# Performance work log

Measured on AMD Instinct MI355X. Metric: run time of the kernel, lower is better.

Reference implementation:

```python
import jax, jax.numpy as jnp
import numpy as np

NL, D, NH, HD, MLP, L = 4, 1280, 16, 80, 5120, 2048
SEG = 512  # patches per packed image


def setup_inputs() -> dict:
    key = jax.random.key(0)
    ks = jax.random.split(key, 16)
    s = 0.02
    # per-segment RoPE frequency table: positions restart at each image boundary
    inv_freq = 1.0 / (10000.0 ** (jnp.arange(0, HD, 2, dtype=jnp.float32) / HD))  # (HD/2,)
    pos = (jnp.arange(L) % SEG).astype(jnp.float32)
    rotary_pos_emb = pos[:, None] * inv_freq[None, :]  # (L, HD/2)
    return {
        "x": jax.random.normal(ks[0], (L, D), jnp.float32),
        "rotary_pos_emb": rotary_pos_emb,
        "cu_seqlens": jnp.array([0, 512, 1024, 1536, 2048], jnp.int32),
        "ln1_g": 1.0 + s * jax.random.normal(ks[1], (NL, D), jnp.float32),
        "ln1_b": s * jax.random.normal(ks[2], (NL, D), jnp.float32),
        "ln2_g": 1.0 + s * jax.random.normal(ks[3], (NL, D), jnp.float32),
        "ln2_b": s * jax.random.normal(ks[4], (NL, D), jnp.float32),
        "qkv_w": s * jax.random.normal(ks[5], (NL, 3 * D, D), jnp.float32),
        "qkv_b": s * jax.random.normal(ks[6], (NL, 3 * D), jnp.float32),
        "proj_w": s * jax.random.normal(ks[7], (NL, D, D), jnp.float32),
        "proj_b": s * jax.random.normal(ks[8], (NL, D), jnp.float32),
        "mlp_w1": s * jax.random.normal(ks[9], (NL, MLP, D), jnp.float32),
        "mlp_b1": s * jax.random.normal(ks[10], (NL, MLP), jnp.float32),
        "mlp_w2": s * jax.random.normal(ks[11], (NL, D, MLP), jnp.float32),
        "mlp_b2": s * jax.random.normal(ks[12], (NL, D), jnp.float32),
    }


def _ln(x, g, b):
    m = jnp.mean(x, axis=-1, keepdims=True)
    v = jnp.mean((x - m) ** 2, axis=-1, keepdims=True)
    return (x - m) * jax.lax.rsqrt(v + 1e-6) * g + b


def _rope(t, cos, sin):
    # t: (L, H, HD); cos/sin: (L, 1, HD)
    half = t.shape[-1] // 2
    rot = jnp.concatenate([-t[..., half:], t[..., :half]], axis=-1)
    return t * cos + rot * sin


def reference(x, rotary_pos_emb, cu_seqlens, ln1_g, ln1_b, ln2_g, ln2_b,
              qkv_w, qkv_b, proj_w, proj_b, mlp_w1, mlp_b1, mlp_w2, mlp_b2):
    Lx = x.shape[0]
    cos = jnp.cos(rotary_pos_emb)
    sin = jnp.sin(rotary_pos_emb)
    cos = jnp.concatenate([cos, cos], axis=-1)[:, None, :]  # (L,1,HD)
    sin = jnp.concatenate([sin, sin], axis=-1)[:, None, :]
    # block-diagonal attention mask from cu_seqlens via segment ids
    seg = jnp.searchsorted(cu_seqlens, jnp.arange(Lx), side="right")  # (L,)
    mask = seg[:, None] == seg[None, :]  # (L,L) bool
    neg = jnp.finfo(jnp.float32).min
    scale = 1.0 / np.sqrt(HD)
    for l in range(qkv_w.shape[0]):
        h = _ln(x, ln1_g[l], ln1_b[l])
        qkv = (h @ qkv_w[l].T + qkv_b[l]).reshape(Lx, 3, NH, HD)
        q, k, v = qkv[:, 0], qkv[:, 1], qkv[:, 2]  # (L,H,HD) each
        q = _rope(q, cos, sin)
        k = _rope(k, cos, sin)
        scores = jnp.einsum("lhd,mhd->hlm", q, k) * scale  # (H,L,L)
        scores = jnp.where(mask[None], scores, neg)
        w = jax.nn.softmax(scores.astype(jnp.float32), axis=-1).astype(x.dtype)
        att = jnp.einsum("hlm,mhd->lhd", w, v).reshape(Lx, NH * HD)
        x = x + att @ proj_w[l].T + proj_b[l]
        h = _ln(x, ln2_g[l], ln2_b[l])
        x = x + jax.nn.gelu(h @ mlp_w1[l].T + mlp_b1[l], approximate=True) @ mlp_w2[l].T + mlp_b2[l]
    return x
```

## Files before the change

kernel.cpp:

```cpp
#include <hip/hip_runtime.h>
#include <cstdint>
#include <cstddef>

typedef unsigned short u16;
typedef __bf16 bf16_t;
typedef bf16_t bf16x8 __attribute__((ext_vector_type(8)));
typedef float f32x4 __attribute__((ext_vector_type(4)));

#define NLAY 4
#define DMODEL 1280
#define NHEAD 16
#define HDIM 80
#define HDP 96
#define MLPD 5120
#define LTOK 2048
#define SEGLEN 512

__device__ __forceinline__ u16 f2bf(float f) {
  union { float f; unsigned u; } x; x.f = f;
  unsigned r = x.u + 0x7fffu + ((x.u >> 16) & 1u);
  return (u16)(r >> 16);
}
__device__ __forceinline__ float bf2f(u16 s) {
  union { unsigned u; float f; } x; x.u = ((unsigned)s) << 16;
  return x.f;
}

#define GLOAD_LDS16(gsrc, ldst) \
  __builtin_amdgcn_global_load_lds((const __attribute__((address_space(1))) void*)(gsrc), \
                                   (__attribute__((address_space(3))) void*)(ldst), 16, 0, 0)

__device__ __forceinline__ void barrier_mem() {
  asm volatile("s_barrier" ::: "memory");
}

#define C0 (3 * DMODEL * DMODEL / 4)
#define C1 (C0 + DMODEL * DMODEL / 4)
#define C2 (C1 + MLPD * DMODEL / 4)
#define C3 (C2 + DMODEL * MLPD / 4)
__global__ __launch_bounds__(256) void cvt4(const float* __restrict__ s_q,
                                            const float* __restrict__ s_p,
                                            const float* __restrict__ s_1,
                                            const float* __restrict__ s_2,
                                            u16* __restrict__ o_q, u16* __restrict__ o_p,
                                            u16* __restrict__ o_1, u16* __restrict__ o_2) {
  int i = blockIdx.x * 256 + threadIdx.x;
  const float* src; u16* dst; int off;
  if (i < C0)      { src = s_q; dst = o_q; off = i; }
  else if (i < C1) { src = s_p; dst = o_p; off = i - C0; }
  else if (i < C2) { src = s_1; dst = o_1; off = i - C1; }
  else if (i < C3) { src = s_2; dst = o_2; off = i - C2; }
  else return;
  const float4 v = reinterpret_cast<const float4*>(src)[off];
  union { u16 s[4]; uint2 u; } o;
  o.s[0] = f2bf(v.x); o.s[1] = f2bf(v.y); o.s[2] = f2bf(v.z); o.s[3] = f2bf(v.w);
  reinterpret_cast<uint2*>(dst)[off] = o.u;
}

__global__ __launch_bounds__(256) void ln_bf16(const float* __restrict__ x,
                                               const float* __restrict__ g,
                                               const float* __restrict__ b,
                                               u16* __restrict__ out) {
  int row = blockIdx.x;
  int t = threadIdx.x;
  const float* xr = x + (size_t)row * DMODEL;
  float v[5]; float s = 0.f, s2 = 0.f;
#pragma unroll
  for (int i = 0; i < 5; i++) { v[i] = xr[t + i * 256]; s += v[i]; s2 += v[i] * v[i]; }
#pragma unroll
  for (int off = 32; off; off >>= 1) { s += __shfl_down(s, off); s2 += __shfl_down(s2, off); }
  __shared__ float ps[4], ps2[4];
  int w = t >> 6;
  if ((t & 63) == 0) { ps[w] = s; ps2[w] = s2; }
  __syncthreads();
  s = ps[0] + ps[1] + ps[2] + ps[3];
  s2 = ps2[0] + ps2[1] + ps2[2] + ps2[3];
  float mean = s * (1.f / DMODEL);
  float var = s2 * (1.f / DMODEL) - mean * mean;
  float inv = rsqrtf(var + 1e-6f);
#pragma unroll
  for (int i = 0; i < 5; i++) {
    int c = t + i * 256;
    out[(size_t)row * DMODEL + c] = f2bf((v[i] - mean) * inv * g[c] + b[c]);
  }
}

template <int EPI>
__global__ __launch_bounds__(512, 4) void gemmhp(const u16* __restrict__ A,
                                                 const u16* __restrict__ B,
                                                 const float* __restrict__ bias,
                                                 u16* __restrict__ Cb,
                                                 int M, int N, int K) {
  __shared__ u16 As[3][128 * 32];
  __shared__ u16 Bs[3][256 * 32];

  int gN = gridDim.x, gM = gridDim.y;
  int flat = blockIdx.x + gN * blockIdx.y;
  int nwg = gN * gM;
  int qc = nwg >> 3, rc = nwg & 7;
  int xcd = flat & 7, pos = flat >> 3;
  int start = (xcd < rc) ? xcd * (qc + 1) : rc * (qc + 1) + (xcd - rc) * qc;
  int swz = start + pos;
  int m0 = (swz % gM) * 128;
  int n0 = (swz / gM) * 256;

  int t = threadIdx.x, lane = t & 63, w = t >> 6;
  int wm = w >> 2, wn = w & 3;
  int r = lane & 15, kq = lane >> 4;
  f32x4 acc[4][4] = {};

  auto stageA = [&](int buf, int k0) {
    int row = t >> 2, s = t & 3;
    int ss = s ^ ((row >> 1) & 3);
    GLOAD_LDS16(A + (size_t)(m0 + row) * K + k0 + ss * 8, &As[buf][t * 8]);
  };
  auto stageB = [&](int buf, int k0) {
#pragma unroll
    for (int i = 0; i < 2; i++) {
      int chunk = i * 512 + t;
      int row = chunk >> 2, s = chunk & 3;
      int ss = s ^ ((row >> 1) & 3);
      GLOAD_LDS16(B + (size_t)(n0 + row) * K + k0 + ss * 8, &Bs[buf][chunk * 8]);
    }
  };

  int NT = K >> 5;
  stageA(0, 0); stageB(0, 0);
  stageA(1, 32); stageB(1, 32);

  int bt = 0;
  for (int kt = 0; kt < NT; kt++) {
    if (kt == NT - 1) asm volatile("s_waitcnt vmcnt(0)" ::: "memory");
    else              asm volatile("s_waitcnt vmcnt(3)" ::: "memory");
    barrier_mem();
    const u16* as = As[bt];
    const u16* bs = Bs[bt];
    int b2 = bt + 2; if (b2 >= 3) b2 -= 3;
    bool st = (kt + 2) < NT;
    int k2 = (kt + 2) << 5;

    bf16x8 af[4], bfv[4];
#pragma unroll
    for (int i = 0; i < 4; i++) {
      int row = wm * 64 + i * 16 + r;
      int ss = kq ^ ((row >> 1) & 3);
      af[i] = *(const bf16x8*)&as[row * 32 + ss * 8];
    }
#pragma unroll
    for (int j = 0; j < 4; j++) {
      int row = wn * 64 + j * 16 + r;
      int ss = kq ^ ((row >> 1) & 3);
      bfv[j] = *(const bf16x8*)&bs[row * 32 + ss * 8];
    }
    if (st) { stageA(b2, k2); stageB(b2, k2); }
    __builtin_amdgcn_s_setprio(1);
#pragma unroll
    for (int i = 0; i < 4; i++)
#pragma unroll
      for (int j = 0; j < 4; j++)
        acc[i][j] = __builtin_amdgcn_mfma_f32_16x16x32_bf16(af[i], bfv[j], acc[i][j], 0, 0, 0);
    __builtin_amdgcn_s_setprio(0);

    bt++; if (bt == 3) bt = 0;
  }

#pragma unroll
  for (int i = 0; i < 4; i++) {
#pragma unroll
    for (int j = 0; j < 4; j++) {
      int col = n0 + wn * 64 + j * 16 + r;
      float bv = bias[col];
#pragma unroll
      for (int reg = 0; reg < 4; reg++) {
        int rowg = m0 + wm * 64 + i * 16 + kq * 4 + reg;
        float val = acc[i][j][reg] + bv;
        if (EPI == 2) {
          float z2 = -1.5957691216057308f * fmaf(0.044715f * val, val * val, val);
          float gg = val / (1.f + __expf(z2));
          Cb[(size_t)rowg * N + col] = f2bf(gg);
        } else {
          Cb[(size_t)rowg * N + col] = f2bf(val);
        }
      }
    }
  }
}

template <int EPI>
__global__ __launch_bounds__(256, 3) void gemmdp(const u16* __restrict__ A,
                                                 const u16* __restrict__ B,
                                                 const float* __restrict__ bias,
                                                 float* __restrict__ Cf,
                                                 int M, int N, int K) {
  __shared__ u16 As[3][128 * 32];
  __shared__ u16 Bs[3][128 * 32];

  int gN = gridDim.x, gM = gridDim.y;
  int flat = blockIdx.x + gN * blockIdx.y;
  int nwg = gN * gM;
  int qc = nwg >> 3, rc = nwg & 7;
  int xcd = flat & 7, pos = flat >> 3;
  int start = (xcd < rc) ? xcd * (qc + 1) : rc * (qc + 1) + (xcd - rc) * qc;
  int swz = start + pos;
  int m0 = (swz % gM) * 128;
  int n0 = (swz / gM) * 128;

  int t = threadIdx.x, lane = t & 63, w = t >> 6;
  int wm = w >> 1, wn = w & 1;
  int r = lane & 15, kq = lane >> 4;
  f32x4 acc[4][4] = {};

  auto stage = [&](int buf, int k0) {
#pragma unroll
    for (int i = 0; i < 2; i++) {
      int chunk = i * 256 + t;
      int row = chunk >> 2, s = chunk & 3;
      int ss = s ^ ((row >> 1) & 3);
      GLOAD_LDS16(A + (size_t)(m0 + row) * K + k0 + ss * 8, &As[buf][chunk * 8]);
    }
#pragma unroll
    for (int i = 0; i < 2; i++) {
      int chunk = i * 256 + t;
      int row = chunk >> 2, s = chunk & 3;
      int ss = s ^ ((row >> 1) & 3);
      GLOAD_LDS16(B + (size_t)(n0 + row) * K + k0 + ss * 8, &Bs[buf][chunk * 8]);
    }
  };

  int NT = K >> 5;
  stage(0, 0);
  stage(1, 32);

  int bt = 0;
  for (int kt = 0; kt < NT; kt++) {
    if (kt == NT - 1) asm volatile("s_waitcnt vmcnt(0)" ::: "memory");
    else              asm volatile("s_waitcnt vmcnt(4)" ::: "memory");
    barrier_mem();
    const u16* as = As[bt];
    const u16* bs = Bs[bt];
    int b2 = bt + 2; if (b2 >= 3) b2 -= 3;
    bool st = (kt + 2) < NT;
    int k2 = (kt + 2) << 5;

    bf16x8 af[4], bfv[4];
#pragma unroll
    for (int i = 0; i < 4; i++) {
      int row = wm * 64 + i * 16 + r;
      int ss = kq ^ ((row >> 1) & 3);
      af[i] = *(const bf16x8*)&as[row * 32 + ss * 8];
    }
#pragma unroll
    for (int j = 0; j < 4; j++) {
      int row = wn * 64 + j * 16 + r;
      int ss = kq ^ ((row >> 1) & 3);
      bfv[j] = *(const bf16x8*)&bs[row * 32 + ss * 8];
    }
    if (st) stage(b2, k2);
    __builtin_amdgcn_s_setprio(1);
#pragma unroll
    for (int i = 0; i < 4; i++)
#pragma unroll
      for (int j = 0; j < 4; j++)
        acc[i][j] = __builtin_amdgcn_mfma_f32_16x16x32_bf16(af[i], bfv[j], acc[i][j], 0, 0, 0);
    __builtin_amdgcn_s_setprio(0);

    bt++; if (bt == 3) bt = 0;
  }

#pragma unroll
  for (int i = 0; i < 4; i++) {
#pragma unroll
    for (int j = 0; j < 4; j++) {
      int col = n0 + wn * 64 + j * 16 + r;
      float bv = bias[col];
#pragma unroll
      for (int reg = 0; reg < 4; reg++) {
        int rowg = m0 + wm * 64 + i * 16 + kq * 4 + reg;
        Cf[(size_t)rowg * N + col] += acc[i][j][reg] + bv;
      }
    }
  }
}

__global__ __launch_bounds__(256) void rope_pack(const u16* __restrict__ qkv,
                                                 const float* __restrict__ rpe,
                                                 u16* __restrict__ qp,
                                                 u16* __restrict__ kp) {
  int l = blockIdx.x;
  int t = threadIdx.x;
  __shared__ float cs[40], sn[40];
  if (t < 40) {
    float a = rpe[l * 40 + t];
    cs[t] = cosf(a);
    sn[t] = sinf(a);
  }
  __syncthreads();
  const u16* row = qkv + (size_t)l * (3 * DMODEL);
  const float scale = 0.11180339887498949f;
#pragma unroll
  for (int i = 0; i < 5; i++) {
    int e = t + i * 256;
    int h = e / HDIM, d = e - h * HDIM;
    int dm = (d < 40) ? d : d - 40;
    float c = cs[dm], s = sn[dm];
    float qv = bf2f(row[h * HDIM + d]);
    float qr = (d < 40) ? -bf2f(row[h * HDIM + d + 40]) : bf2f(row[h * HDIM + d - 40]);
    qp[((size_t)h * LTOK + l) * HDP + d] = f2bf((qv * c + qr * s) * scale);
    float kv = bf2f(row[DMODEL + h * HDIM + d]);
    float kr = (d < 40) ? -bf2f(row[DMODEL + h * HDIM + d + 40]) : bf2f(row[DMODEL + h * HDIM + d - 40]);
    kp[((size_t)h * LTOK + l) * HDP + d] = f2bf(kv * c + kr * s);
  }
  {
    int h = t >> 4, p = t & 15;
    qp[((size_t)h * LTOK + l) * HDP + HDIM + p] = 0;
    kp[((size_t)h * LTOK + l) * HDP + HDIM + p] = 0;
  }
}

__global__ __launch_bounds__(256) void vtrans(const u16* __restrict__ qkv,
                                              u16* __restrict__ vt) {
  int blk = blockIdx.x;
  int h = blk >> 5, lt = blk & 31;
  int t = threadIdx.x;
  __shared__ u16 ld[64][81];
#pragma unroll
  for (int i = 0; i < 20; i++) {
    int idx = t + i * 256;
    int ll = idx / HDIM, d = idx - ll * HDIM;
    ld[ll][d] = qkv[(size_t)(lt * 64 + ll) * (3 * DMODEL) + 2 * DMODEL + h * HDIM + d];
  }
  __syncthreads();
#pragma unroll
  for (int i = 0; i < 20; i++) {
    int idx = t + i * 256;
    int d = idx >> 6, ll = idx & 63;
    vt[((size_t)h * HDIM + d) * LTOK + lt * 64 + ll] = ld[ll][d];
  }
}

__global__ __launch_bounds__(256) void attn(const u16* __restrict__ qp,
                                            const u16* __restrict__ kp,
                                            const u16* __restrict__ vt,
                                            u16* __restrict__ out) {
  int bid = blockIdx.x;
  int h = bid >> 5;
  int seg = (bid >> 3) & 3;
  int qt = bid & 7;
  int t = threadIdx.x, w = t >> 6, lane = t & 63;
  int r = lane & 15, kq = lane >> 4;
  __shared__ u16 P[4][16][512];
  int seg0 = seg * SEGLEN;
  int q0 = seg0 + qt * 64 + w * 16;

  bf16x8 qf[3];
  const u16* qrow = qp + ((size_t)h * LTOK + q0 + r) * HDP;
#pragma unroll
  for (int kk = 0; kk < 3; kk++) qf[kk] = *(const bf16x8*)(qrow + kk * 32 + kq * 8);

  f32x4 sc[32];
#pragma unroll
  for (int j = 0; j < 32; j++) {
    f32x4 a = {0.f, 0.f, 0.f, 0.f};
    const u16* krow = kp + ((size_t)h * LTOK + seg0 + j * 16 + r) * HDP;
#pragma unroll
    for (int kk = 0; kk < 3; kk++) {
      bf16x8 bfr = *(const bf16x8*)(krow + kk * 32 + kq * 8);
      a = __builtin_amdgcn_mfma_f32_16x16x32_bf16(qf[kk], bfr, a, 0, 0, 0);
    }
    sc[j] = a;
  }

#pragma unroll
  for (int rr = 0; rr < 4; rr++) {
    float m = -1e30f;
#pragma unroll
    for (int j = 0; j < 32; j++) m = fmaxf(m, sc[j][rr]);
#pragma unroll
    for (int off = 1; off < 16; off <<= 1) m = fmaxf(m, __shfl_xor(m, off));
    float s = 0.f;
#pragma unroll
    for (int j = 0; j < 32; j++) { float e = __expf(sc[j][rr] - m); sc[j][rr] = e; s += e; }
#pragma unroll
    for (int off = 1; off < 16; off <<= 1) s += __shfl_xor(s, off);
    float inv = 1.f / s;
#pragma unroll
    for (int j = 0; j < 32; j++)
      P[w][kq * 4 + rr][j * 16 + r] = f2bf(sc[j][rr] * inv);
  }
  __syncthreads();

  f32x4 oc[5] = {};
#pragma unroll
  for (int tt = 0; tt < 16; tt++) {
    bf16x8 a = *(const bf16x8*)&P[w][r][tt * 32 + kq * 8];
#pragma unroll
    for (int n = 0; n < 5; n++) {
      const u16* vrow = vt + ((size_t)h * HDIM + n * 16 + r) * LTOK + seg0 + tt * 32 + kq * 8;
      bf16x8 bfr = *(const bf16x8*)vrow;
      oc[n] = __builtin_amdgcn_mfma_f32_16x16x32_bf16(a, bfr, oc[n], 0, 0, 0);
    }
  }
#pragma unroll
  for (int n = 0; n < 5; n++)
#pragma unroll
    for (int reg = 0; reg < 4; reg++) {
      int l = q0 + kq * 4 + reg;
      out[(size_t)l * DMODEL + h * HDIM + n * 16 + r] = f2bf(oc[n][reg]);
    }
}

extern "C" void kernel_launch(void* const* d_in, const int* in_sizes, int n_in,
                              void* d_out, int out_size, void* d_ws, size_t ws_size,
                              hipStream_t stream) {
  (void)in_sizes; (void)n_in; (void)out_size; (void)ws_size;
  const float* x_in   = (const float*)d_in[0];
  const float* rpe    = (const float*)d_in[1];
  const float* ln1_g  = (const float*)d_in[3];
  const float* ln1_b  = (const float*)d_in[4];
  const float* ln2_g  = (const float*)d_in[5];
  const float* ln2_b  = (const float*)d_in[6];
  const float* qkv_w  = (const float*)d_in[7];
  const float* qkv_b  = (const float*)d_in[8];
  const float* proj_w = (const float*)d_in[9];
  const float* proj_b = (const float*)d_in[10];
  const float* mlp_w1 = (const float*)d_in[11];
  const float* mlp_b1 = (const float*)d_in[12];
  const float* mlp_w2 = (const float*)d_in[13];
  const float* mlp_b2 = (const float*)d_in[14];
  float* x = (float*)d_out;

  char* ws = (char*)d_ws;
  size_t off = 0;
  auto alloc = [&](size_t bytes) -> char* {
    char* p = ws + off;
    off = (off + bytes + 255) & ~(size_t)255;
    return p;
  };
  u16* wq  = (u16*)alloc((size_t)3 * DMODEL * DMODEL * 2);
  u16* wp  = (u16*)alloc((size_t)DMODEL * DMODEL * 2);
  u16* w1  = (u16*)alloc((size_t)MLPD * DMODEL * 2);
  u16* w2  = (u16*)alloc((size_t)DMODEL * MLPD * 2);
  u16* hb  = (u16*)alloc((size_t)LTOK * DMODEL * 2);
  u16* qkvb = (u16*)alloc((size_t)LTOK * 3 * DMODEL * 2);
  u16* qp  = (u16*)alloc((size_t)NHEAD * LTOK * HDP * 2);
  u16* kp  = (u16*)alloc((size_t)NHEAD * LTOK * HDP * 2);
  u16* vt  = (u16*)alloc((size_t)NHEAD * HDIM * LTOK * 2);
  u16* att = (u16*)alloc((size_t)LTOK * DMODEL * 2);
  u16* ge  = (u16*)alloc((size_t)LTOK * MLPD * 2);

  hipMemcpyAsync(x, x_in, (size_t)LTOK * DMODEL * sizeof(float),
                 hipMemcpyDeviceToDevice, stream);

  for (int l = 0; l < NLAY; l++) {
    cvt4<<<(C3 + 255) / 256, 256, 0, stream>>>(
        qkv_w + (size_t)l * 3 * DMODEL * DMODEL, proj_w + (size_t)l * DMODEL * DMODEL,
        mlp_w1 + (size_t)l * MLPD * DMODEL, mlp_w2 + (size_t)l * DMODEL * MLPD,
        wq, wp, w1, w2);

    ln_bf16<<<LTOK, 256, 0, stream>>>(x, ln1_g + l * DMODEL, ln1_b + l * DMODEL, hb);
    gemmhp<3><<<dim3(15, 16), 512, 0, stream>>>(
        hb, wq, qkv_b + (size_t)l * 3 * DMODEL, qkvb, LTOK, 3 * DMODEL, DMODEL);
    rope_pack<<<LTOK, 256, 0, stream>>>(qkvb, rpe, qp, kp);
    vtrans<<<NHEAD * 32, 256, 0, stream>>>(qkvb, vt);
    attn<<<NHEAD * 4 * 8, 256, 0, stream>>>(qp, kp, vt, att);
    gemmdp<1><<<dim3(10, 16), 256, 0, stream>>>(
        att, wp, proj_b + (size_t)l * DMODEL, x, LTOK, DMODEL, DMODEL);
    ln_bf16<<<LTOK, 256, 0, stream>>>(x, ln2_g + l * DMODEL, ln2_b + l * DMODEL, hb);
    gemmhp<2><<<dim3(20, 16), 512, 0, stream>>>(
        hb, w1, mlp_b1 + (size_t)l * MLPD, ge, LTOK, MLPD, DMODEL);
    gemmdp<1><<<dim3(10, 16), 256, 0, stream>>>(
        ge, w2, mlp_b2 + (size_t)l * DMODEL, x, LTOK, DMODEL, MLPD);
  }
}
```

Before: 1.078 ms.

## Split-K the projection and MLP-down GEMMs with bf16 partials and a reduce kernel

Replaces the residual-accumulating GEMM used for the attention projection and the MLP down-projection with a split-K variant. It launches 4 K-slices per tile, so 640 workgroups run instead of 160 on a 256-CU part. Each slice writes its partial sums as bf16 into reused scratch buffers (the ge region, and the hb region spilling into qkvb). A separate vectorised kernel then sums the four partials, adds the bias and updates the fp32 residual. The cost is extra memory traffic and one more launch per GEMM, plus reduced precision because the partials are rounded to bf16 before summation.

New measurement: 927.7 us. -13.9%, faster.

```diff
diff --git a/kernel.cpp b/kernel.cpp
--- a/kernel.cpp
+++ b/kernel.cpp
@@ -186,12 +186,10 @@
   }
 }
 
-template <int EPI>
-__global__ __launch_bounds__(256, 3) void gemmdp(const u16* __restrict__ A,
-                                                 const u16* __restrict__ B,
-                                                 const float* __restrict__ bias,
-                                                 float* __restrict__ Cf,
-                                                 int M, int N, int K) {
+__global__ __launch_bounds__(256, 3) void gemmskb(const u16* __restrict__ A,
+                                                  const u16* __restrict__ B,
+                                                  u16* __restrict__ P,
+                                                  int M, int N, int K, int KC) {
   __shared__ u16 As[3][128 * 32];
   __shared__ u16 Bs[3][128 * 32];
 
@@ -204,6 +202,8 @@
   int swz = start + pos;
   int m0 = (swz % gM) * 128;
   int n0 = (swz / gM) * 128;
+  int kbase = blockIdx.z * KC;
+  u16* Pz = P + (size_t)blockIdx.z * M * N;
 
   int t = threadIdx.x, lane = t & 63, w = t >> 6;
   int wm = w >> 1, wn = w & 1;
@@ -227,9 +227,9 @@
     }
   };
 
-  int NT = K >> 5;
-  stage(0, 0);
-  stage(1, 32);
+  int NT = KC >> 5;
+  stage(0, kbase);
+  stage(1, kbase + 32);
 
   int bt = 0;
   for (int kt = 0; kt < NT; kt++) {
@@ -240,7 +240,7 @@
     const u16* bs = Bs[bt];
     int b2 = bt + 2; if (b2 >= 3) b2 -= 3;
     bool st = (kt + 2) < NT;
-    int k2 = (kt + 2) << 5;
+    int k2 = kbase + ((kt + 2) << 5);
 
     bf16x8 af[4], bfv[4];
 #pragma unroll
@@ -272,14 +272,39 @@
 #pragma unroll
     for (int j = 0; j < 4; j++) {
       int col = n0 + wn * 64 + j * 16 + r;
-      float bv = bias[col];
 #pragma unroll
       for (int reg = 0; reg < 4; reg++) {
         int rowg = m0 + wm * 64 + i * 16 + kq * 4 + reg;
-        Cf[(size_t)rowg * N + col] += acc[i][j][reg] + bv;
+        Pz[(size_t)rowg * N + col] = f2bf(acc[i][j][reg]);
       }
     }
   }
+}
+
+#define N8TOT (LTOK * DMODEL / 8)
+__global__ __launch_bounds__(256) void reduce4b(const u16* __restrict__ P,
+                                                const float* __restrict__ bias,
+                                                float4* __restrict__ x) {
+  int i = blockIdx.x * 256 + threadIdx.x;
+  if (i >= N8TOT) return;
+  const size_t PS = (size_t)LTOK * DMODEL;
+  float s[8] = {};
+#pragma unroll
+  for (int z = 0; z < 4; z++) {
+    uint4 pv = *reinterpret_cast<const uint4*>(P + z * PS + (size_t)i * 8);
+    const u16* ps = (const u16*)&pv;
+#pragma unroll
+    for (int e = 0; e < 8; e++) s[e] += bf2f(ps[e]);
+  }
+  int cb = (i % (DMODEL / 8)) * 8;
+  float4 b0 = *reinterpret_cast<const float4*>(bias + cb);
+  float4 b1 = *reinterpret_cast<const float4*>(bias + cb + 4);
+  float4 xv0 = x[i * 2], xv1 = x[i * 2 + 1];
+  xv0.x += s[0] + b0.x; xv0.y += s[1] + b0.y;
+  xv0.z += s[2] + b0.z; xv0.w += s[3] + b0.w;
+  xv1.x += s[4] + b1.x; xv1.y += s[5] + b1.y;
+  xv1.z += s[6] + b1.z; xv1.w += s[7] + b1.w;
+  x[i * 2] = xv0; x[i * 2 + 1] = xv1;
 }
 
 __global__ __launch_bounds__(256) void rope_pack(const u16* __restrict__ qkv,
@@ -447,6 +472,8 @@
   u16* vt  = (u16*)alloc((size_t)NHEAD * HDIM * LTOK * 2);
   u16* att = (u16*)alloc((size_t)LTOK * DMODEL * 2);
   u16* ge  = (u16*)alloc((size_t)LTOK * MLPD * 2);
+  u16* pk_proj = ge;
+  u16* pk_mlp2 = hb;
 
   hipMemcpyAsync(x, x_in, (size_t)LTOK * DMODEL * sizeof(float),
                  hipMemcpyDeviceToDevice, stream);
@@ -463,12 +490,16 @@
     rope_pack<<<LTOK, 256, 0, stream>>>(qkvb, rpe, qp, kp);
     vtrans<<<NHEAD * 32, 256, 0, stream>>>(qkvb, vt);
     attn<<<NHEAD * 4 * 8, 256, 0, stream>>>(qp, kp, vt, att);
-    gemmdp<1><<<dim3(10, 16), 256, 0, stream>>>(
-        att, wp, proj_b + (size_t)l * DMODEL, x, LTOK, DMODEL, DMODEL);
+    gemmskb<<<dim3(10, 16, 4), 256, 0, stream>>>(
+        att, wp, pk_proj, LTOK, DMODEL, DMODEL, DMODEL / 4);
+    reduce4b<<<(N8TOT + 255) / 256, 256, 0, stream>>>(
+        pk_proj, proj_b + (size_t)l * DMODEL, (float4*)x);
     ln_bf16<<<LTOK, 256, 0, stream>>>(x, ln2_g + l * DMODEL, ln2_b + l * DMODEL, hb);
     gemmhp<2><<<dim3(20, 16), 512, 0, stream>>>(
         hb, w1, mlp_b1 + (size_t)l * MLPD, ge, LTOK, MLPD, DMODEL);
-    gemmdp<1><<<dim3(10, 16), 256, 0, stream>>>(
-        ge, w2, mlp_b2 + (size_t)l * DMODEL, x, LTOK, DMODEL, MLPD);
-  }
-}
+    gemmskb<<<dim3(10, 16, 4), 256, 0, stream>>>(
+        ge, w2, pk_mlp2, LTOK, DMODEL, MLPD, MLPD / 4);
+    reduce4b<<<(N8TOT + 255) / 256, 256, 0, stream>>>(
+        pk_mlp2, mlp_b2 + (size_t)l * DMODEL, (float4*)x);
+  }
+}
```
